# Kernel tuning notes

Hardware: AMD Instinct MI355X
Metric: run time of the kernel (lower is better)

The kernel has to match this reference:

```python
import jax, jax.numpy as jnp
import numpy as np

DIM = 64
SQRT_DIM = np.sqrt(DIM).astype(np.float32)
NEG_INF = -1e9


def setup_inputs() -> dict:
    key = jax.random.key(0)
    kq, kk, kv, km = jax.random.split(key, 4)
    B, Q, K, D = 32, 1024, 1024, DIM
    query = jax.random.normal(kq, (B, Q, D), dtype=jnp.float32)
    k = jax.random.normal(kk, (B, K, D), dtype=jnp.float32)
    value = jax.random.normal(kv, (B, K, D), dtype=jnp.float32)
    mask = jax.random.randint(km, (B, Q, K), 0, 2).astype(jnp.bool_)
    return {"query": query, "key": k, "value": value, "mask": mask}


def reference(query, key, value, mask):
    # score: [B, Q, K]
    score = jnp.einsum('bqd,bkd->bqk', query, key) / SQRT_DIM
    score = jnp.where(mask, NEG_INF, score)
    attn = jax.nn.softmax(score, axis=-1)
    context = jnp.einsum('bqk,bkd->bqd', attn, value)
    return (context, attn)
```

## Files before the change

kernel.cpp:

```cpp
#include <hip/hip_runtime.h>

constexpr int BATCH = 32;
constexpr int QLEN  = 1024;
constexpr int KLEN  = 1024;
constexpr int DIM   = 64;
constexpr int TQ    = 16;

typedef float    f32x4 __attribute__((ext_vector_type(4)));
typedef int      i32x4 __attribute__((ext_vector_type(4)));
typedef _Float16 f16x8 __attribute__((ext_vector_type(8)));
typedef _Float16 f16x4 __attribute__((ext_vector_type(4)));
typedef unsigned long long u64;
typedef unsigned int u32;

__device__ __forceinline__ f16x8 cvt_h8(f32x4 a, f32x4 b) {
  f16x8 h;
  h[0] = (_Float16)a[0]; h[1] = (_Float16)a[1]; h[2] = (_Float16)a[2]; h[3] = (_Float16)a[3];
  h[4] = (_Float16)b[0]; h[5] = (_Float16)b[1]; h[6] = (_Float16)b[2]; h[7] = (_Float16)b[3];
  return h;
}

constexpr int TK = 128;
__global__ __launch_bounds__(256)
void vtkh_kernel(const float* __restrict__ V, const float* __restrict__ Kg,
                 _Float16* __restrict__ Vt, _Float16* __restrict__ Kh) {
  __shared__ _Float16 lt[DIM][TK + 8];
  const int b = blockIdx.y, k0 = blockIdx.x * TK;
  const int t = threadIdx.x;
  const int d4 = (t & 15) * 4;
  #pragma unroll
  for (int p = 0; p < TK / 16; ++p) {
    const int kl = (t >> 4) + p * 16;
    const f32x4 v = *(const f32x4*)(V + ((size_t)(b * KLEN + k0 + kl)) * DIM + d4);
    #pragma unroll
    for (int j = 0; j < 4; ++j) lt[d4 + j][kl] = (_Float16)v[j];
  }
  #pragma unroll
  for (int p = 0; p < 8; ++p) {
    const int idx = t + p * 256;
    const int kl = idx >> 4, dd = (idx & 15) * 4;
    const f32x4 v = *(const f32x4*)(Kg + ((size_t)(b * KLEN + k0 + kl)) * DIM + dd);
    f16x4 h = { (_Float16)v[0], (_Float16)v[1], (_Float16)v[2], (_Float16)v[3] };
    *(f16x4*)(Kh + ((size_t)(b * KLEN + k0 + kl)) * DIM + dd) = h;
  }
  __syncthreads();
  const int d = t >> 2;
  #pragma unroll
  for (int j2 = 0; j2 < TK / 32; ++j2) {
    const int seg = (t & 3) + j2 * 4;
    *(f16x8*)(Vt + (size_t)b * DIM * KLEN + (size_t)d * KLEN + k0 + seg * 8) =
        *(const f16x8*)(&lt[d][seg * 8]);
  }
}

__global__ __launch_bounds__(256, 4)
void sdpa_kernel(const float* __restrict__ Qg, const _Float16* __restrict__ Kh,
                 const _Float16* __restrict__ Vt, const int* __restrict__ Mg,
                 float* __restrict__ Ctx, float* __restrict__ Attn)
{
  __shared__ float rs[4][16];
  __shared__ __attribute__((aligned(16))) _Float16 sp[TQ * 1024];

  const int tid  = threadIdx.x;
  const int w    = tid >> 6;
  const int l    = tid & 63;
  const int n16  = l & 15;
  const int quad = l >> 4;
  char* const spb = (char*)sp;

  const int lin = blockIdx.x;
  const int b   = lin >> 6;
  const int q0  = (lin & 63) * TQ;

  const int* mrow = Mg + ((size_t)(b * QLEN + q0 + n16)) * KLEN + w * 256 + quad * 4;

  i32x4 mv[16];
  #pragma unroll
  for (int tt = 0; tt < 16; ++tt)
    mv[tt] = __builtin_nontemporal_load((const i32x4*)(mrow + tt * 16));

  const float qscl = 0.125f * 1.44269504f;
  const float* qb = Qg + ((size_t)(b * QLEN + q0 + n16)) * DIM + quad * 8;
  f32x4 qa0 = *(const f32x4*)(qb),      qa1 = *(const f32x4*)(qb + 4);
  f32x4 qa2 = *(const f32x4*)(qb + 32), qa3 = *(const f32x4*)(qb + 36);
  #pragma unroll
  for (int i = 0; i < 4; ++i) { qa0[i] *= qscl; qa1[i] *= qscl; qa2[i] *= qscl; qa3[i] *= qscl; }
  const f16x8 aq0 = cvt_h8(qa0, qa1);
  const f16x8 aq1 = cvt_h8(qa2, qa3);

  const _Float16* kb = Kh + (size_t)b * KLEN * DIM + quad * 8;

  f32x4 rsum4 = {0.f, 0.f, 0.f, 0.f};
  #pragma unroll
  for (int tt = 0; tt < 16; ++tt) {
    const _Float16* kp = kb + (size_t)((w * 16 + tt) * 16 + n16) * DIM;
    const f16x8 ak0 = *(const f16x8*)(kp);
    const f16x8 ak1 = *(const f16x8*)(kp + 32);
    f32x4 acc = {0.f, 0.f, 0.f, 0.f};
    acc = __builtin_amdgcn_mfma_f32_16x16x32_f16(ak0, aq0, acc, 0, 0, 0);
    acc = __builtin_amdgcn_mfma_f32_16x16x32_f16(ak1, aq1, acc, 0, 0, 0);
    f16x4 ph;
    #pragma unroll
    for (int i = 0; i < 4; ++i) {
      const float e = mv[tt][i] ? 0.f : __builtin_amdgcn_exp2f(acc[i]);
      rsum4[i] += e;
      ph[i] = (_Float16)e;
    }
    const int g = w * 64 + tt * 4 + quad;
    *(f16x4*)(spb + (n16 << 11) + ((g * 8) ^ ((n16 & 7) << 4))) = ph;
  }
  float rsum = (rsum4[0] + rsum4[1]) + (rsum4[2] + rsum4[3]);
  rsum += __shfl_xor(rsum, 16, 64);
  rsum += __shfl_xor(rsum, 32, 64);
  if (quad == 0) rs[w][n16] = rsum;
  __syncthreads();

  #pragma unroll
  for (int rr = 0; rr < 4; ++rr) {
    const int row = w * 4 + rr;
    const float invr =
        __builtin_amdgcn_rcpf(rs[0][row] + rs[1][row] + rs[2][row] + rs[3][row]);
    float* arow = Attn + ((size_t)(b * QLEN + q0 + row)) * KLEN;
    #pragma unroll
    for (int j = 0; j < 4; ++j) {
      const int g = j * 64 + l;
      const f16x4 hv = *(const f16x4*)(spb + (row << 11) + ((g * 8) ^ ((row & 7) << 4)));
      f32x4 ov = { (float)hv[0] * invr, (float)hv[1] * invr,
                   (float)hv[2] * invr, (float)hv[3] * invr };
      *(f32x4*)(arow + j * 256 + l * 4) = ov;
    }
  }

  const _Float16* vtb = Vt + ((size_t)(b * DIM + w * 16 + n16)) * KLEN;
  f32x4 c0 = {0.f, 0.f, 0.f, 0.f}, c1 = {0.f, 0.f, 0.f, 0.f};
  #pragma unroll 8
  for (int m = 0; m < 32; m += 2) {
    const int ga = m * 8 + quad * 2;
    const f16x8 pa0 = *(const f16x8*)(spb + (n16 << 11) + ((ga * 8) ^ ((n16 & 7) << 4)));
    const f16x8 pa1 = *(const f16x8*)(spb + (n16 << 11) + (((ga + 8) * 8) ^ ((n16 & 7) << 4)));
    const f16x8 bv0 = *(const f16x8*)(vtb + m * 32 + quad * 8);
    const f16x8 bv1 = *(const f16x8*)(vtb + (m + 1) * 32 + quad * 8);
    c0 = __builtin_amdgcn_mfma_f32_16x16x32_f16(bv0, pa0, c0, 0, 0, 0);
    c1 = __builtin_amdgcn_mfma_f32_16x16x32_f16(bv1, pa1, c1, 0, 0, 0);
  }
  const float invq =
      __builtin_amdgcn_rcpf(rs[0][n16] + rs[1][n16] + rs[2][n16] + rs[3][n16]);
  f32x4 cv = { (c0[0] + c1[0]) * invq, (c0[1] + c1[1]) * invq,
               (c0[2] + c1[2]) * invq, (c0[3] + c1[3]) * invq };
  *(f32x4*)(Ctx + ((size_t)(b * QLEN + q0 + n16)) * DIM + w * 16 + quad * 4) = cv;
}

extern "C" void kernel_launch(void* const* d_in, const int* in_sizes, int n_in,
                              void* d_out, int out_size, void* d_ws, size_t ws_size,
                              hipStream_t stream) {
  const float* Qg = (const float*)d_in[0];
  const float* Kg = (const float*)d_in[1];
  const float* Vg = (const float*)d_in[2];
  const int*   Mg = (const int*)d_in[3];
  float* Ctx  = (float*)d_out;
  float* Attn = (float*)d_out + (size_t)BATCH * QLEN * DIM;
  _Float16* Vt = (_Float16*)d_ws;
  _Float16* Kh = (_Float16*)((char*)d_ws + (size_t)BATCH * DIM * KLEN * 2);

  dim3 tgrid(KLEN / TK, BATCH);
  vtkh_kernel<<<tgrid, 256, 0, stream>>>(Vg, Kg, Vt, Kh);

  sdpa_kernel<<<2048, 256, 0, stream>>>(Qg, Kh, Vt, Mg, Ctx, Attn);
}
```

Baseline: 309.5 us.

## Make SDPA blocks process four tiles with double-buffered LDS pipelining

```diff
diff --git a/kernel.cpp b/kernel.cpp
--- a/kernel.cpp
+++ b/kernel.cpp
@@ -53,101 +53,119 @@
   }
 }
 
-__global__ __launch_bounds__(256, 4)
+__global__ __launch_bounds__(256, 2)
 void sdpa_kernel(const float* __restrict__ Qg, const _Float16* __restrict__ Kh,
                  const _Float16* __restrict__ Vt, const int* __restrict__ Mg,
                  float* __restrict__ Ctx, float* __restrict__ Attn)
 {
-  __shared__ float rs[4][16];
-  __shared__ __attribute__((aligned(16))) _Float16 sp[TQ * 1024];
+  __shared__ float rs[2][4][16];
+  __shared__ __attribute__((aligned(16))) _Float16 sp[2][TQ * 1024];
 
   const int tid  = threadIdx.x;
   const int w    = tid >> 6;
   const int l    = tid & 63;
   const int n16  = l & 15;
   const int quad = l >> 4;
-  char* const spb = (char*)sp;
 
-  const int lin = blockIdx.x;
-  const int b   = lin >> 6;
-  const int q0  = (lin & 63) * TQ;
-
-  const int* mrow = Mg + ((size_t)(b * QLEN + q0 + n16)) * KLEN + w * 256 + quad * 4;
+  const int base = blockIdx.x * 4;
 
   i32x4 mv[16];
+
+  auto loadMask = [&](int lin) {
+    const int b = lin >> 6, q0 = (lin & 63) * TQ;
+    const int* mrow = Mg + ((size_t)(b * QLEN + q0 + n16)) * KLEN + w * 256 + quad * 4;
+    #pragma unroll
+    for (int tt = 0; tt < 16; ++tt)
+      mv[tt] = __builtin_nontemporal_load((const i32x4*)(mrow + tt * 16));
+  };
+
+  auto computeA = [&](int lin, int buf) {
+    const int b = lin >> 6, q0 = (lin & 63) * TQ;
+    char* const spb = (char*)&sp[buf][0];
+    const float qscl = 0.125f * 1.44269504f;
+    const float* qb = Qg + ((size_t)(b * QLEN + q0 + n16)) * DIM + quad * 8;
+    f32x4 qa0 = *(const f32x4*)(qb),      qa1 = *(const f32x4*)(qb + 4);
+    f32x4 qa2 = *(const f32x4*)(qb + 32), qa3 = *(const f32x4*)(qb + 36);
+    #pragma unroll
+    for (int i = 0; i < 4; ++i) { qa0[i] *= qscl; qa1[i] *= qscl; qa2[i] *= qscl; qa3[i] *= qscl; }
+    const f16x8 aq0 = cvt_h8(qa0, qa1);
+    const f16x8 aq1 = cvt_h8(qa2, qa3);
+    const _Float16* kb = Kh + (size_t)b * KLEN * DIM + quad * 8;
+    f32x4 rsum4 = {0.f, 0.f, 0.f, 0.f};
+    #pragma unroll
+    for (int tt = 0; tt < 16; ++tt) {
+      const _Float16* kp = kb + (size_t)((w * 16 + tt) * 16 + n16) * DIM;
+      const f16x8 ak0 = *(const f16x8*)(kp);
+      const f16x8 ak1 = *(const f16x8*)(kp + 32);
+      f32x4 acc = {0.f, 0.f, 0.f, 0.f};
+      acc = __builtin_amdgcn_mfma_f32_16x16x32_f16(ak0, aq0, acc, 0, 0, 0);
+      acc = __builtin_amdgcn_mfma_f32_16x16x32_f16(ak1, aq1, acc, 0, 0, 0);
+      f16x4 ph;
+      #pragma unroll
+      for (int i = 0; i < 4; ++i) {
+        const float e = mv[tt][i] ? 0.f : __builtin_amdgcn_exp2f(acc[i]);
+        rsum4[i] += e;
+        ph[i] = (_Float16)e;
+      }
+      const int g = w * 64 + tt * 4 + quad;
+      *(f16x4*)(spb + (n16 << 11) + ((g * 8) ^ ((n16 & 7) << 4))) = ph;
+    }
+    float rsum = (rsum4[0] + rsum4[1]) + (rsum4[2] + rsum4[3]);
+    rsum += __shfl_xor(rsum, 16, 64);
+    rsum += __shfl_xor(rsum, 32, 64);
+    if (quad == 0) rs[buf][w][n16] = rsum;
+  };
+
+  auto passC = [&](int lin, int buf) {
+    const int b = lin >> 6, q0 = (lin & 63) * TQ;
+    char* const spb = (char*)&sp[buf][0];
+    #pragma unroll
+    for (int rr = 0; rr < 4; ++rr) {
+      const int row = w * 4 + rr;
+      const float invr = __builtin_amdgcn_rcpf(
+          rs[buf][0][row] + rs[buf][1][row] + rs[buf][2][row] + rs[buf][3][row]);
+      float* arow = Attn + ((size_t)(b * QLEN + q0 + row)) * KLEN;
+      #pragma unroll
+      for (int j = 0; j < 4; ++j) {
+        const int g = j * 64 + l;
+        const f16x4 hv = *(const f16x4*)(spb + (row << 11) + ((g * 8) ^ ((row & 7) << 4)));
+        f32x4 ov = { (float)hv[0] * invr, (float)hv[1] * invr,
+                     (float)hv[2] * invr, (float)hv[3] * invr };
+        *(f32x4*)(arow + j * 256 + l * 4) = ov;
+      }
+    }
+    const _Float16* vtb = Vt + ((size_t)(b * DIM + w * 16 + n16)) * KLEN;
+    f32x4 c0 = {0.f, 0.f, 0.f, 0.f}, c1 = {0.f, 0.f, 0.f, 0.f};
+    #pragma unroll 8
+    for (int m = 0; m < 32; m += 2) {
+      const int ga = m * 8 + quad * 2;
+      const f16x8 pa0 = *(const f16x8*)(spb + (n16 << 11) + ((ga * 8) ^ ((n16 & 7) << 4)));
+      const f16x8 pa1 = *(const f16x8*)(spb + (n16 << 11) + (((ga + 8) * 8) ^ ((n16 & 7) << 4)));
+      const f16x8 bv0 = *(const f16x8*)(vtb + m * 32 + quad * 8);
+      const f16x8 bv1 = *(const f16x8*)(vtb + (m + 1) * 32 + quad * 8);
+      c0 = __builtin_amdgcn_mfma_f32_16x16x32_f16(bv0, pa0, c0, 0, 0, 0);
+      c1 = __builtin_amdgcn_mfma_f32_16x16x32_f16(bv1, pa1, c1, 0, 0, 0);
+    }
+    const float invq = __builtin_amdgcn_rcpf(
+        rs[buf][0][n16] + rs[buf][1][n16] + rs[buf][2][n16] + rs[buf][3][n16]);
+    f32x4 cv = { (c0[0] + c1[0]) * invq, (c0[1] + c1[1]) * invq,
+                 (c0[2] + c1[2]) * invq, (c0[3] + c1[3]) * invq };
+    *(f32x4*)(Ctx + ((size_t)(b * QLEN + q0 + n16)) * DIM + w * 16 + quad * 4) = cv;
+  };
+
+  loadMask(base);
+  computeA(base, 0);
+  __syncthreads();
   #pragma unroll
-  for (int tt = 0; tt < 16; ++tt)
-    mv[tt] = __builtin_nontemporal_load((const i32x4*)(mrow + tt * 16));
-
-  const float qscl = 0.125f * 1.44269504f;
-  const float* qb = Qg + ((size_t)(b * QLEN + q0 + n16)) * DIM + quad * 8;
-  f32x4 qa0 = *(const f32x4*)(qb),      qa1 = *(const f32x4*)(qb + 4);
-  f32x4 qa2 = *(const f32x4*)(qb + 32), qa3 = *(const f32x4*)(qb + 36);
-  #pragma unroll
-  for (int i = 0; i < 4; ++i) { qa0[i] *= qscl; qa1[i] *= qscl; qa2[i] *= qscl; qa3[i] *= qscl; }
-  const f16x8 aq0 = cvt_h8(qa0, qa1);
-  const f16x8 aq1 = cvt_h8(qa2, qa3);
-
-  const _Float16* kb = Kh + (size_t)b * KLEN * DIM + quad * 8;
-
-  f32x4 rsum4 = {0.f, 0.f, 0.f, 0.f};
-  #pragma unroll
-  for (int tt = 0; tt < 16; ++tt) {
-    const _Float16* kp = kb + (size_t)((w * 16 + tt) * 16 + n16) * DIM;
-    const f16x8 ak0 = *(const f16x8*)(kp);
-    const f16x8 ak1 = *(const f16x8*)(kp + 32);
-    f32x4 acc = {0.f, 0.f, 0.f, 0.f};
-    acc = __builtin_amdgcn_mfma_f32_16x16x32_f16(ak0, aq0, acc, 0, 0, 0);
-    acc = __builtin_amdgcn_mfma_f32_16x16x32_f16(ak1, aq1, acc, 0, 0, 0);
-    f16x4 ph;
-    #pragma unroll
-    for (int i = 0; i < 4; ++i) {
-      const float e = mv[tt][i] ? 0.f : __builtin_amdgcn_exp2f(acc[i]);
-      rsum4[i] += e;
-      ph[i] = (_Float16)e;
-    }
-    const int g = w * 64 + tt * 4 + quad;
-    *(f16x4*)(spb + (n16 << 11) + ((g * 8) ^ ((n16 & 7) << 4))) = ph;
-  }
-  float rsum = (rsum4[0] + rsum4[1]) + (rsum4[2] + rsum4[3]);
-  rsum += __shfl_xor(rsum, 16, 64);
-  rsum += __shfl_xor(rsum, 32, 64);
-  if (quad == 0) rs[w][n16] = rsum;
-  __syncthreads();
-
-  #pragma unroll
-  for (int rr = 0; rr < 4; ++rr) {
-    const int row = w * 4 + rr;
-    const float invr =
-        __builtin_amdgcn_rcpf(rs[0][row] + rs[1][row] + rs[2][row] + rs[3][row]);
-    float* arow = Attn + ((size_t)(b * QLEN + q0 + row)) * KLEN;
-    #pragma unroll
-    for (int j = 0; j < 4; ++j) {
-      const int g = j * 64 + l;
-      const f16x4 hv = *(const f16x4*)(spb + (row << 11) + ((g * 8) ^ ((row & 7) << 4)));
-      f32x4 ov = { (float)hv[0] * invr, (float)hv[1] * invr,
-                   (float)hv[2] * invr, (float)hv[3] * invr };
-      *(f32x4*)(arow + j * 256 + l * 4) = ov;
+  for (int t = 0; t < 4; ++t) {
+    const int cur = t & 1;
+    if (t < 3) loadMask(base + t + 1);
+    passC(base + t, cur);
+    if (t < 3) {
+      computeA(base + t + 1, cur ^ 1);
+      __syncthreads();
     }
   }
-
-  const _Float16* vtb = Vt + ((size_t)(b * DIM + w * 16 + n16)) * KLEN;
-  f32x4 c0 = {0.f, 0.f, 0.f, 0.f}, c1 = {0.f, 0.f, 0.f, 0.f};
-  #pragma unroll 8
-  for (int m = 0; m < 32; m += 2) {
-    const int ga = m * 8 + quad * 2;
-    const f16x8 pa0 = *(const f16x8*)(spb + (n16 << 11) + ((ga * 8) ^ ((n16 & 7) << 4)));
-    const f16x8 pa1 = *(const f16x8*)(spb + (n16 << 11) + (((ga + 8) * 8) ^ ((n16 & 7) << 4)));
-    const f16x8 bv0 = *(const f16x8*)(vtb + m * 32 + quad * 8);
-    const f16x8 bv1 = *(const f16x8*)(vtb + (m + 1) * 32 + quad * 8);
-    c0 = __builtin_amdgcn_mfma_f32_16x16x32_f16(bv0, pa0, c0, 0, 0, 0);
-    c1 = __builtin_amdgcn_mfma_f32_16x16x32_f16(bv1, pa1, c1, 0, 0, 0);
-  }
-  const float invq =
-      __builtin_amdgcn_rcpf(rs[0][n16] + rs[1][n16] + rs[2][n16] + rs[3][n16]);
-  f32x4 cv = { (c0[0] + c1[0]) * invq, (c0[1] + c1[1]) * invq,
-               (c0[2] + c1[2]) * invq, (c0[3] + c1[3]) * invq };
-  *(f32x4*)(Ctx + ((size_t)(b * QLEN + q0 + n16)) * DIM + w * 16 + quad * 4) = cv;
 }
 
 extern "C" void kernel_launch(void* const* d_in, const int* in_sizes, int n_in,
@@ -165,5 +183,5 @@
   dim3 tgrid(KLEN / TK, BATCH);
   vtkh_kernel<<<tgrid, 256, 0, stream>>>(Vg, Kg, Vt, Kh);
 
-  sdpa_kernel<<<2048, 256, 0, stream>>>(Qg, Kh, Vt, Mg, Ctx, Attn);
+  sdpa_kernel<<<512, 256, 0, stream>>>(Qg, Kh, Vt, Mg, Ctx, Attn);
 }
```

Result: no change. 308.3 us (-0.4%).
